# Optimization experiments

Measured on AMD Instinct MI355X. Metric: run time of the kernel, lower is better.

## Reference

```python
import jax, jax.numpy as jnp
import numpy as np

B_SZ, L, H, P = 8, 8192, 1024, 64  # batch, seq, d_inner, ssm_size
CONJ_SYM = True
DT_MIN, DT_MAX, DT_FLOOR = 1e-3, 1e-1, 1e-4


def setup_inputs() -> dict:
    key = jax.random.key(0)
    ks = jax.random.split(key, 8)
    u = jax.random.normal(ks[0], (B_SZ, L, H), dtype=jnp.float32)
    h_real = jnp.zeros((B_SZ, P), dtype=jnp.float32)
    h_imag = jnp.zeros((B_SZ, P), dtype=jnp.float32)
    # HiPPO-like stable init: Re(Lambda) = -0.5, Im(Lambda) = pi*k
    A_real = -0.5 * jnp.ones((P,), dtype=jnp.float32)
    A_imag = jnp.pi * jnp.arange(P, dtype=jnp.float32)
    local_P = 2 * P if CONJ_SYM else P
    b_scale = np.sqrt(1.0 / local_P).astype(np.float32)
    c_scale = np.sqrt(1.0 / H).astype(np.float32)
    B_real = jax.random.normal(ks[1], (P, H), dtype=jnp.float32) * b_scale
    B_imag = jax.random.normal(ks[2], (P, H), dtype=jnp.float32) * b_scale
    C_real = jax.random.normal(ks[3], (H, P), dtype=jnp.float32) * c_scale
    C_imag = jax.random.normal(ks[4], (H, P), dtype=jnp.float32) * c_scale
    D = jax.random.normal(ks[5], (H,), dtype=jnp.float32)
    # torch init: dt = exp(U(log dt_min, log dt_max)).clamp(dt_floor); inv_dt = dt + log(-expm1(-dt))
    log_dt = jax.random.uniform(ks[6], (P,), dtype=jnp.float32) \
        * (np.log(DT_MAX) - np.log(DT_MIN)) + np.log(DT_MIN)
    dt0 = jnp.clip(jnp.exp(log_dt), DT_FLOOR, None)
    inv_dt = dt0 + jnp.log(-jnp.expm1(-dt0))
    return {"u": u, "h_real": h_real, "h_imag": h_imag,
            "A_real": A_real, "A_imag": A_imag,
            "B_real": B_real, "B_imag": B_imag,
            "C_real": C_real, "C_imag": C_imag,
            "D": D, "inv_dt": inv_dt}


def reference(u, h_real, h_imag, A_real, A_imag, B_real, B_imag,
              C_real, C_imag, D, inv_dt):
    A = A_real + 1j * A_imag            # (P,)
    Bm = B_real + 1j * B_imag           # (P, H)
    Cm = C_real + 1j * C_imag           # (H, P)
    dt = jax.nn.softplus(inv_dt)        # step_rescale = 1.0
    # bilinear discretization
    den = 1.0 - (dt / 2.0) * A
    dA = (1.0 + (dt / 2.0) * A) / den   # (P,)
    dB = (dt / den)[:, None] * Bm       # (P, H)
    # input projection: Bu[b,l,p] = sum_h dB[p,h] * u[b,l,h]
    Bu = jnp.einsum('blh,ph->blp', u, dB)              # complex64 (B, L, P)
    h0 = h_real + 1j * h_imag                          # (B, P)
    Bu = Bu.at[:, 0].add(dA * h0)                      # fold initial state in
    a = jnp.broadcast_to(dA, Bu.shape)
    def combine(e1, e2):
        a1, b1 = e1
        a2, b2 = e2
        return a2 * a1, a2 * b1 + b2
    _, hs = jax.lax.associative_scan(combine, (a, Bu), axis=1)  # (B, L, P)
    yc = jnp.einsum('blp,hp->blh', hs, Cm)
    scale = 2.0 if CONJ_SYM else 1.0
    y = scale * yc.real + D * u
    h_last = hs[:, -1]
    return y, h_last.real, h_last.imag
```

## Files before the change

kernel.cpp:

```cpp
#include <hip/hip_runtime.h>

typedef unsigned short ushort_t;
typedef short s8v __attribute__((ext_vector_type(8)));
typedef unsigned short ushort8 __attribute__((ext_vector_type(8)));
typedef float floatx4 __attribute__((ext_vector_type(4)));

#define MFMA16(a, b, c) __builtin_amdgcn_mfma_f32_16x16x32_bf16((a), (b), (c), 0, 0, 0)

static constexpr int B_SZ = 8;
static constexpr int L = 8192;
static constexpr int H = 1024;
static constexpr int M_TOT = B_SZ * L;
static constexpr int S_CH = 128;
static constexpr int NC = L / S_CH;

__device__ inline ushort_t f2bf(float f) {
    union { float f; unsigned u; } v; v.f = f;
    unsigned r = v.u + 0x7fffu + ((v.u >> 16) & 1u);
    return (ushort_t)(r >> 16);
}

__global__ void params_kernel(const float* __restrict__ A_real,
                              const float* __restrict__ A_imag,
                              const float* __restrict__ inv_dt,
                              float* __restrict__ params,
                              float* __restrict__ dApow) {
    int p = threadIdx.x;
    float x = inv_dt[p];
    float dt = (x > 20.f) ? x : log1pf(expf(x));
    float ar = A_real[p], ai = A_imag[p];
    float dr = 1.f - 0.5f * dt * ar;
    float di = -0.5f * dt * ai;
    float inv = 1.f / fmaf(dr, dr, di * di);
    float nr = 1.f + 0.5f * dt * ar, ni = 0.5f * dt * ai;
    float dAr = (nr * dr + ni * di) * inv;
    float dAi = (ni * dr - nr * di) * inv;
    params[p]       = dAr;
    params[64 + p]  = dAi;
    params[128 + p] = dt * dr * inv;
    params[192 + p] = -dt * di * inv;
    float pr = 1.f, pi = 0.f;
    dApow[2 * p] = 1.f; dApow[2 * p + 1] = 0.f;
    for (int k = 1; k <= S_CH; k++) {
        float npr = pr * dAr - pi * dAi;
        float npi = pr * dAi + pi * dAr;
        pr = npr; pi = npi;
        dApow[k * 128 + 2 * p]     = pr;
        dApow[k * 128 + 2 * p + 1] = pi;
    }
}

__global__ void build_w(const float* __restrict__ Br, const float* __restrict__ Bi,
                        const float* __restrict__ Cr, const float* __restrict__ Ci,
                        const float* __restrict__ params,
                        ushort_t* __restrict__ W1T, ushort_t* __restrict__ CeffT) {
    int t = blockIdx.x * 256 + threadIdx.x;
    if (t < 128 * 1024) {
        int n = t >> 10, k = t & 1023;
        int p = n >> 1;
        float sr = params[128 + p], si = params[192 + p];
        float br = Br[p * 1024 + k], bi = Bi[p * 1024 + k];
        float v = (n & 1) ? (sr * bi + si * br) : (sr * br - si * bi);
        W1T[t] = f2bf(v);
    } else {
        int t2 = t - 128 * 1024;
        int h = t2 >> 7, k = t2 & 127;
        int p = k >> 1;
        float v = (k & 1) ? -2.f * Ci[h * 64 + p] : 2.f * Cr[h * 64 + p];
        CeffT[t2] = f2bf(v);
    }
}

__global__ __launch_bounds__(256) void gemm1s(const float* __restrict__ u,
                                              const ushort_t* __restrict__ W1T,
                                              const float* __restrict__ params,
                                              const float* __restrict__ dApow,
                                              float* __restrict__ hloc,
                                              float* __restrict__ endbuf) {
    __shared__ float bus[128 * 128];
    ushort_t* As = (ushort_t*)bus;
    ushort_t* Bs = As + 128 * 40;
    int tid = threadIdx.x;
    int wave = tid >> 6, lane = tid & 63;
    int q = lane >> 4, mn = lane & 15;
    size_t row0 = (size_t)blockIdx.x * 128;
    int r = tid >> 1, half = tid & 1;

    floatx4 acc[2][8] = {};

    for (int kk = 0; kk < 1024; kk += 32) {
        __syncthreads();
        {
            const float4* up = (const float4*)(u + (row0 + r) * 1024 + kk + half * 16);
            float4 f0 = up[0], f1 = up[1], f2 = up[2], f3 = up[3];
            ushort8 t0, t1;
            t0[0] = f2bf(f0.x); t0[1] = f2bf(f0.y); t0[2] = f2bf(f0.z); t0[3] = f2bf(f0.w);
            t0[4] = f2bf(f1.x); t0[5] = f2bf(f1.y); t0[6] = f2bf(f1.z); t0[7] = f2bf(f1.w);
            t1[0] = f2bf(f2.x); t1[1] = f2bf(f2.y); t1[2] = f2bf(f2.z); t1[3] = f2bf(f2.w);
            t1[4] = f2bf(f3.x); t1[5] = f2bf(f3.y); t1[6] = f2bf(f3.z); t1[7] = f2bf(f3.w);
            ushort8* dst = (ushort8*)&As[r * 40 + half * 16];
            dst[0] = t0; dst[1] = t1;
            const ushort8* wp = (const ushort8*)(W1T + r * 1024 + kk + half * 16);
            ushort8* db = (ushort8*)&Bs[r * 40 + half * 16];
            db[0] = wp[0]; db[1] = wp[1];
        }
        __syncthreads();
        s8v a0 = *(const s8v*)&As[(wave * 32 + mn) * 40 + q * 8];
        s8v a1 = *(const s8v*)&As[(wave * 32 + 16 + mn) * 40 + q * 8];
        #pragma unroll
        for (int j = 0; j < 8; j++) {
            s8v bf = *(const s8v*)&Bs[(j * 16 + mn) * 40 + q * 8];
            acc[0][j] = MFMA16(a0, bf, acc[0][j]);
            acc[1][j] = MFMA16(a1, bf, acc[1][j]);
        }
    }
    __syncthreads();
    #pragma unroll
    for (int i = 0; i < 2; i++)
        #pragma unroll
        for (int j = 0; j < 8; j++)
            #pragma unroll
            for (int reg = 0; reg < 4; reg++) {
                int row = wave * 32 + i * 16 + q * 4 + reg;
                bus[row * 128 + j * 16 + mn] = acc[i][j][reg];
            }
    __syncthreads();

    float dAr = params[lane], dAi = params[64 + lane];
    float hr = 0.f, hi = 0.f;
    int base = wave * 32 * 128 + 2 * lane;
    #pragma unroll 4
    for (int t = 0; t < 32; t++) {
        float2 v = *(float2*)&bus[base + t * 128];
        float nhr = fmaf(dAr, hr, fmaf(-dAi, hi, v.x));
        float nhi = fmaf(dAr, hi, fmaf(dAi, hr, v.y));
        hr = nhr; hi = nhi;
        *(float2*)&bus[base + t * 128] = make_float2(hr, hi);
    }
    __syncthreads();

    float a32r = dApow[32 * 128 + 2 * lane], a32i = dApow[32 * 128 + 2 * lane + 1];
    float cr = 0.f, ci = 0.f;
    for (int w2 = 0; w2 < wave; w2++) {
        float2 e = *(float2*)&bus[(w2 * 32 + 31) * 128 + 2 * lane];
        float tr = fmaf(a32r, cr, fmaf(-a32i, ci, e.x));
        float ti = fmaf(a32r, ci, fmaf(a32i, cr, e.y));
        cr = tr; ci = ti;
    }

    float* gbase = hloc + (row0 + wave * 32) * 128 + 2 * lane;
    float lr = 0.f, li = 0.f;
    #pragma unroll 4
    for (int t = 0; t < 32; t++) {
        float2 v = *(float2*)&bus[base + t * 128];
        float pr = dApow[(t + 1) * 128 + 2 * lane];
        float pi = dApow[(t + 1) * 128 + 2 * lane + 1];
        float orr = v.x + pr * cr - pi * ci;
        float oi  = v.y + pr * ci + pi * cr;
        *(float2*)(gbase + (size_t)t * 128) = make_float2(orr, oi);
        lr = orr; li = oi;
    }
    if (wave == 3) {
        float* e = endbuf + (size_t)blockIdx.x * 128 + 2 * lane;
        e[0] = lr; e[1] = li;
    }
}

__global__ void scan_carry(const float* __restrict__ endbuf,
                           const float* __restrict__ dApow,
                           const float* __restrict__ h0r,
                           const float* __restrict__ h0i,
                           float* __restrict__ carry) {
    int t = blockIdx.x * 64 + threadIdx.x;
    int b = t >> 6, p = t & 63;
    float aSr = dApow[S_CH * 128 + 2 * p], aSi = dApow[S_CH * 128 + 2 * p + 1];
    float cr = h0r[b * 64 + p], ci = h0i[b * 64 + p];
    for (int c = 0; c < NC; c++) {
        float* dst = carry + ((size_t)b * NC + c) * 128 + 2 * p;
        dst[0] = cr; dst[1] = ci;
        const float* e = endbuf + ((size_t)b * NC + c) * 128 + 2 * p;
        float er = e[0], ei = e[1];
        float nr = fmaf(aSr, cr, fmaf(-aSi, ci, er));
        float ni = fmaf(aSr, ci, fmaf(aSi, cr, ei));
        cr = nr; ci = ni;
    }
}

__global__ __launch_bounds__(256) void gemm2(const float* __restrict__ hloc,
                                             const ushort_t* __restrict__ CeffT,
                                             const float* __restrict__ u,
                                             const float* __restrict__ D,
                                             const float* __restrict__ dApow,
                                             const float* __restrict__ carry,
                                             float* __restrict__ y,
                                             float* __restrict__ out_hlast) {
    __shared__ ushort_t As[128][136];
    __shared__ ushort_t Bs[128][136];
    int tid = threadIdx.x;
    int wave = tid >> 6, lane = tid & 63;
    int q = lane >> 4, mn = lane & 15;
    size_t row0 = (size_t)blockIdx.x * 128;
    int r = tid >> 1, half = tid & 1;
    {
        size_t rrow = row0 + r;
        int b = (int)(rrow >> 13);
        int l = (int)(rrow & (L - 1));
        int c = l >> 7;
        int kp = (l & (S_CH - 1)) + 1;
        const float4* hp = (const float4*)(hloc + rrow * 128 + half * 64);
        const float4* pw = (const float4*)(dApow + (size_t)kp * 128 + half * 64);
        const float4* cv = (const float4*)(carry + ((size_t)b * NC + c) * 128 + half * 64);
        ushort8* dst = (ushort8*)&As[r][half * 64];
        bool last = (l == L - 1);
        #pragma unroll
        for (int j = 0; j < 8; j++) {
            float4 hv0 = hp[2 * j], hv1 = hp[2 * j + 1];
            float4 p0 = pw[2 * j], p1 = pw[2 * j + 1];
            float4 c0 = cv[2 * j], c1 = cv[2 * j + 1];
            float r0 = hv0.x + p0.x * c0.x - p0.y * c0.y;
            float i0 = hv0.y + p0.x * c0.y + p0.y * c0.x;
            float r1 = hv0.z + p0.z * c0.z - p0.w * c0.w;
            float i1 = hv0.w + p0.z * c0.w + p0.w * c0.z;
            float r2 = hv1.x + p1.x * c1.x - p1.y * c1.y;
            float i2 = hv1.y + p1.x * c1.y + p1.y * c1.x;
            float r3 = hv1.z + p1.z * c1.z - p1.w * c1.w;
            float i3 = hv1.w + p1.z * c1.w + p1.w * c1.z;
            ushort8 o;
            o[0] = f2bf(r0); o[1] = f2bf(i0); o[2] = f2bf(r1); o[3] = f2bf(i1);
            o[4] = f2bf(r2); o[5] = f2bf(i2); o[6] = f2bf(r3); o[7] = f2bf(i3);
            dst[j] = o;
            if (last) {
                int pb = (half * 64 + j * 8) >> 1;
                out_hlast[b * 64 + pb]           = r0; out_hlast[512 + b * 64 + pb]     = i0;
                out_hlast[b * 64 + pb + 1]       = r1; out_hlast[512 + b * 64 + pb + 1] = i1;
                out_hlast[b * 64 + pb + 2]       = r2; out_hlast[512 + b * 64 + pb + 2] = i2;
                out_hlast[b * 64 + pb + 3]       = r3; out_hlast[512 + b * 64 + pb + 3] = i3;
            }
        }
    }
    for (int ct = 0; ct < 8; ct++) {
        __syncthreads();
        {
            const ushort8* src = (const ushort8*)(CeffT + (size_t)(ct * 128 + r) * 128 + half * 64);
            ushort8* dst = (ushort8*)&Bs[r][half * 64];
            #pragma unroll
            for (int i = 0; i < 8; i++) dst[i] = src[i];
        }
        __syncthreads();
        floatx4 acc[2][8] = {};
        #pragma unroll
        for (int kk = 0; kk < 128; kk += 32) {
            s8v a0 = *(const s8v*)&As[wave * 32 + mn][kk + q * 8];
            s8v a1 = *(const s8v*)&As[wave * 32 + 16 + mn][kk + q * 8];
            #pragma unroll
            for (int j = 0; j < 8; j++) {
                s8v bf = *(const s8v*)&Bs[j * 16 + mn][kk + q * 8];
                acc[0][j] = MFMA16(a0, bf, acc[0][j]);
                acc[1][j] = MFMA16(a1, bf, acc[1][j]);
            }
        }
        float dv[8];
        #pragma unroll
        for (int j = 0; j < 8; j++) dv[j] = D[ct * 128 + j * 16 + mn];
        #pragma unroll
        for (int i = 0; i < 2; i++)
            #pragma unroll
            for (int j = 0; j < 8; j++) {
                int col = ct * 128 + j * 16 + mn;
                #pragma unroll
                for (int reg = 0; reg < 4; reg++) {
                    size_t row = row0 + wave * 32 + i * 16 + q * 4 + reg;
                    y[row * 1024 + col] = acc[i][j][reg] + dv[j] * u[row * 1024 + col];
                }
            }
    }
}

extern "C" void kernel_launch(void* const* d_in, const int* in_sizes, int n_in,
                              void* d_out, int out_size, void* d_ws, size_t ws_size,
                              hipStream_t stream) {
    const float* u      = (const float*)d_in[0];
    const float* h_r    = (const float*)d_in[1];
    const float* h_i    = (const float*)d_in[2];
    const float* A_real = (const float*)d_in[3];
    const float* A_imag = (const float*)d_in[4];
    const float* B_real = (const float*)d_in[5];
    const float* B_imag = (const float*)d_in[6];
    const float* C_real = (const float*)d_in[7];
    const float* C_imag = (const float*)d_in[8];
    const float* D      = (const float*)d_in[9];
    const float* inv_dt = (const float*)d_in[10];
    float* out = (float*)d_out;

    float* wsf       = (float*)d_ws;
    float* P_params  = wsf;
    float* P_dApow   = wsf + 1024;
    float* P_carry   = wsf + 1024 + 16640;
    float* P_end     = P_carry + 65536;
    ushort_t* P_W1T  = (ushort_t*)(P_end + 65536);
    ushort_t* P_Ceff = P_W1T + 128 * 1024;
    float* P_Bu      = (float*)(P_Ceff + 1024 * 128);

    params_kernel<<<1, 64, 0, stream>>>(A_real, A_imag, inv_dt, P_params, P_dApow);
    build_w<<<1024, 256, 0, stream>>>(B_real, B_imag, C_real, C_imag, P_params, P_W1T, P_Ceff);
    gemm1s<<<M_TOT / 128, 256, 0, stream>>>(u, P_W1T, P_params, P_dApow, P_Bu, P_end);
    scan_carry<<<8, 64, 0, stream>>>(P_end, P_dApow, h_r, h_i, P_carry);
    gemm2<<<M_TOT / 128, 256, 0, stream>>>(P_Bu, P_Ceff, u, D, P_dApow, P_carry,
                                           out, out + (size_t)M_TOT * H);
}
```

Measured before the change: 592.2 us.

## Stage GEMM weights via direct global-to-LDS loads with swizzled prepacked layout

Prepacks the W1T and CeffT weight matrices into a tiled, XOR-swizzled layout. Both GEMMs then bring them into a 64KB LDS buffer with global_load_lds in 4 phases instead of 32 or 8 small per-iteration stages. A-operands (u in gemm1, the corrected hidden state in gemm2) are loaded straight from global into registers and converted with packed bf16 conversion, so they no longer pass through LDS. This removes most barriers and LDS round-trips. The cost is higher register pressure, uncoalesced per-lane A loads, and larger LDS use that may cut occupancy.

```diff
diff --git a/kernel.cpp b/kernel.cpp
--- a/kernel.cpp
+++ b/kernel.cpp
@@ -18,6 +18,20 @@
     union { float f; unsigned u; } v; v.f = f;
     unsigned r = v.u + 0x7fffu + ((v.u >> 16) & 1u);
     return (ushort_t)(r >> 16);
+}
+
+__device__ inline unsigned cvtpk(float lo, float hi) {
+    unsigned r;
+    asm("v_cvt_pk_bf16_f32 %0, %1, %2" : "=v"(r) : "v"(lo), "v"(hi));
+    return r;
+}
+
+typedef union { s8v v; unsigned u[4]; } u32x4;
+
+__device__ inline void gload_lds16(const void* g, void* l) {
+    __builtin_amdgcn_global_load_lds(
+        (const __attribute__((address_space(1))) void*)g,
+        (__attribute__((address_space(3))) void*)l, 16, 0, 0);
 }
 
 __global__ void params_kernel(const float* __restrict__ A_real,
@@ -55,19 +69,39 @@
                         const float* __restrict__ params,
                         ushort_t* __restrict__ W1T, ushort_t* __restrict__ CeffT) {
     int t = blockIdx.x * 256 + threadIdx.x;
-    if (t < 128 * 1024) {
-        int n = t >> 10, k = t & 1023;
+    if (t < 16384) {
+        int ti = t >> 9, g = t & 511;
+        int n = g >> 2;
+        int qq = (g & 3) ^ ((n >> 1) & 3);
+        int kb = ti * 32 + qq * 8;
         int p = n >> 1;
         float sr = params[128 + p], si = params[192 + p];
-        float br = Br[p * 1024 + k], bi = Bi[p * 1024 + k];
-        float v = (n & 1) ? (sr * bi + si * br) : (sr * br - si * bi);
-        W1T[t] = f2bf(v);
+        ushort8 o;
+        #pragma unroll
+        for (int e = 0; e < 8; e++) {
+            int k = kb + e;
+            float br = Br[p * 1024 + k], bi = Bi[p * 1024 + k];
+            float v = (n & 1) ? (sr * bi + si * br) : (sr * br - si * bi);
+            o[e] = f2bf(v);
+        }
+        *(ushort8*)&W1T[t * 8] = o;
     } else {
-        int t2 = t - 128 * 1024;
-        int h = t2 >> 7, k = t2 & 127;
-        int p = k >> 1;
-        float v = (k & 1) ? -2.f * Ci[h * 64 + p] : 2.f * Cr[h * 64 + p];
-        CeffT[t2] = f2bf(v);
+        int t2 = t - 16384;
+        int ct_ti = t2 >> 9, g = t2 & 511;
+        int ct = ct_ti >> 2, ti = ct_ti & 3;
+        int n = g >> 2;
+        int h = ct * 128 + n;
+        int qq = (g & 3) ^ ((n >> 1) & 3);
+        int kb = ti * 32 + qq * 8;
+        ushort8 o;
+        #pragma unroll
+        for (int e = 0; e < 8; e++) {
+            int k = kb + e;
+            int p = k >> 1;
+            float v = (k & 1) ? -2.f * Ci[h * 64 + p] : 2.f * Cr[h * 64 + p];
+            o[e] = f2bf(v);
+        }
+        *(ushort8*)&CeffT[t2 * 8] = o;
     }
 }
 
@@ -77,41 +111,49 @@
                                               const float* __restrict__ dApow,
                                               float* __restrict__ hloc,
                                               float* __restrict__ endbuf) {
-    __shared__ float bus[128 * 128];
-    ushort_t* As = (ushort_t*)bus;
-    ushort_t* Bs = As + 128 * 40;
+    __shared__ ushort_t Blds[32768];
+    float* bus = (float*)Blds;
     int tid = threadIdx.x;
     int wave = tid >> 6, lane = tid & 63;
     int q = lane >> 4, mn = lane & 15;
+    int swz = q ^ ((mn >> 1) & 3);
     size_t row0 = (size_t)blockIdx.x * 128;
-    int r = tid >> 1, half = tid & 1;
+
+    const float* uA0 = u + (row0 + wave * 32 + mn) * 1024 + q * 8;
+    const float* uA1 = uA0 + 16 * 1024;
 
     floatx4 acc[2][8] = {};
 
-    for (int kk = 0; kk < 1024; kk += 32) {
+    for (int ph = 0; ph < 4; ph++) {
+        if (ph) __syncthreads();
+        {
+            const ushort_t* gsrc = W1T + (size_t)ph * 32768 + wave * 512 + lane * 8;
+            ushort_t* ldst = Blds + wave * 512;
+            #pragma unroll
+            for (int it = 0; it < 16; it++)
+                gload_lds16(gsrc + it * 2048, ldst + it * 2048);
+        }
         __syncthreads();
-        {
-            const float4* up = (const float4*)(u + (row0 + r) * 1024 + kk + half * 16);
-            float4 f0 = up[0], f1 = up[1], f2 = up[2], f3 = up[3];
-            ushort8 t0, t1;
-            t0[0] = f2bf(f0.x); t0[1] = f2bf(f0.y); t0[2] = f2bf(f0.z); t0[3] = f2bf(f0.w);
-            t0[4] = f2bf(f1.x); t0[5] = f2bf(f1.y); t0[6] = f2bf(f1.z); t0[7] = f2bf(f1.w);
-            t1[0] = f2bf(f2.x); t1[1] = f2bf(f2.y); t1[2] = f2bf(f2.z); t1[3] = f2bf(f2.w);
-            t1[4] = f2bf(f3.x); t1[5] = f2bf(f3.y); t1[6] = f2bf(f3.z); t1[7] = f2bf(f3.w);
-            ushort8* dst = (ushort8*)&As[r * 40 + half * 16];
-            dst[0] = t0; dst[1] = t1;
-            const ushort8* wp = (const ushort8*)(W1T + r * 1024 + kk + half * 16);
-            ushort8* db = (ushort8*)&Bs[r * 40 + half * 16];
-            db[0] = wp[0]; db[1] = wp[1];
-        }
-        __syncthreads();
-        s8v a0 = *(const s8v*)&As[(wave * 32 + mn) * 40 + q * 8];
-        s8v a1 = *(const s8v*)&As[(wave * 32 + 16 + mn) * 40 + q * 8];
-        #pragma unroll
-        for (int j = 0; j < 8; j++) {
-            s8v bf = *(const s8v*)&Bs[(j * 16 + mn) * 40 + q * 8];
-            acc[0][j] = MFMA16(a0, bf, acc[0][j]);
-            acc[1][j] = MFMA16(a1, bf, acc[1][j]);
+        const float* ua0 = uA0 + ph * 256;
+        const float* ua1 = uA1 + ph * 256;
+        #pragma unroll
+        for (int kt = 0; kt < 8; kt++) {
+            float4 f00 = *(const float4*)(ua0 + kt * 32);
+            float4 f01 = *(const float4*)(ua0 + kt * 32 + 4);
+            float4 f10 = *(const float4*)(ua1 + kt * 32);
+            float4 f11 = *(const float4*)(ua1 + kt * 32 + 4);
+            u32x4 pa0, pa1;
+            pa0.u[0] = cvtpk(f00.x, f00.y); pa0.u[1] = cvtpk(f00.z, f00.w);
+            pa0.u[2] = cvtpk(f01.x, f01.y); pa0.u[3] = cvtpk(f01.z, f01.w);
+            pa1.u[0] = cvtpk(f10.x, f10.y); pa1.u[1] = cvtpk(f10.z, f10.w);
+            pa1.u[2] = cvtpk(f11.x, f11.y); pa1.u[3] = cvtpk(f11.z, f11.w);
+            int bofs = kt * 4096 + swz * 8;
+            #pragma unroll
+            for (int j = 0; j < 8; j++) {
+                s8v bf = *(const s8v*)&Blds[bofs + (j * 16 + mn) * 32];
+                acc[0][j] = MFMA16(pa0.v, bf, acc[0][j]);
+                acc[1][j] = MFMA16(pa1.v, bf, acc[1][j]);
+            }
         }
     }
     __syncthreads();
@@ -129,7 +171,7 @@
     float dAr = params[lane], dAi = params[64 + lane];
     float hr = 0.f, hi = 0.f;
     int base = wave * 32 * 128 + 2 * lane;
-    #pragma unroll 4
+    #pragma unroll 8
     for (int t = 0; t < 32; t++) {
         float2 v = *(float2*)&bus[base + t * 128];
         float nhr = fmaf(dAr, hr, fmaf(-dAi, hi, v.x));
@@ -150,7 +192,7 @@
 
     float* gbase = hloc + (row0 + wave * 32) * 128 + 2 * lane;
     float lr = 0.f, li = 0.f;
-    #pragma unroll 4
+    #pragma unroll 8
     for (int t = 0; t < 32; t++) {
         float2 v = *(float2*)&bus[base + t * 128];
         float pr = dApow[(t + 1) * 128 + 2 * lane];
@@ -194,85 +236,92 @@
                                              const float* __restrict__ carry,
                                              float* __restrict__ y,
                                              float* __restrict__ out_hlast) {
-    __shared__ ushort_t As[128][136];
-    __shared__ ushort_t Bs[128][136];
+    __shared__ ushort_t Blds[32768];
     int tid = threadIdx.x;
     int wave = tid >> 6, lane = tid & 63;
     int q = lane >> 4, mn = lane & 15;
+    int swz = q ^ ((mn >> 1) & 3);
     size_t row0 = (size_t)blockIdx.x * 128;
-    int r = tid >> 1, half = tid & 1;
-    {
-        size_t rrow = row0 + r;
-        int b = (int)(rrow >> 13);
-        int l = (int)(rrow & (L - 1));
-        int c = l >> 7;
-        int kp = (l & (S_CH - 1)) + 1;
-        const float4* hp = (const float4*)(hloc + rrow * 128 + half * 64);
-        const float4* pw = (const float4*)(dApow + (size_t)kp * 128 + half * 64);
-        const float4* cv = (const float4*)(carry + ((size_t)b * NC + c) * 128 + half * 64);
-        ushort8* dst = (ushort8*)&As[r][half * 64];
-        bool last = (l == L - 1);
-        #pragma unroll
-        for (int j = 0; j < 8; j++) {
-            float4 hv0 = hp[2 * j], hv1 = hp[2 * j + 1];
-            float4 p0 = pw[2 * j], p1 = pw[2 * j + 1];
-            float4 c0 = cv[2 * j], c1 = cv[2 * j + 1];
-            float r0 = hv0.x + p0.x * c0.x - p0.y * c0.y;
-            float i0 = hv0.y + p0.x * c0.y + p0.y * c0.x;
-            float r1 = hv0.z + p0.z * c0.z - p0.w * c0.w;
-            float i1 = hv0.w + p0.z * c0.w + p0.w * c0.z;
-            float r2 = hv1.x + p1.x * c1.x - p1.y * c1.y;
-            float i2 = hv1.y + p1.x * c1.y + p1.y * c1.x;
-            float r3 = hv1.z + p1.z * c1.z - p1.w * c1.w;
-            float i3 = hv1.w + p1.z * c1.w + p1.w * c1.z;
-            ushort8 o;
-            o[0] = f2bf(r0); o[1] = f2bf(i0); o[2] = f2bf(r1); o[3] = f2bf(i1);
-            o[4] = f2bf(r2); o[5] = f2bf(i2); o[6] = f2bf(r3); o[7] = f2bf(i3);
-            dst[j] = o;
+    int b = blockIdx.x >> 6;
+    int c = blockIdx.x & 63;
+
+    u32x4 A[2][4];
+    #pragma unroll
+    for (int i = 0; i < 2; i++) {
+        int r_i = wave * 32 + i * 16 + mn;
+        int kp = r_i + 1;
+        const float* hrow = hloc + (row0 + r_i) * 128;
+        const float* prow = dApow + (size_t)kp * 128;
+        const float* crow = carry + ((size_t)b * NC + c) * 128;
+        bool last = (c == NC - 1) && (r_i == 127);
+        #pragma unroll
+        for (int kt = 0; kt < 4; kt++) {
+            int kb = kt * 32 + q * 8;
+            float4 h0 = *(const float4*)(hrow + kb);
+            float4 h1 = *(const float4*)(hrow + kb + 4);
+            float4 p0 = *(const float4*)(prow + kb);
+            float4 p1 = *(const float4*)(prow + kb + 4);
+            float4 c0 = *(const float4*)(crow + kb);
+            float4 c1 = *(const float4*)(crow + kb + 4);
+            float f0 = h0.x + p0.x * c0.x - p0.y * c0.y;
+            float f1 = h0.y + p0.x * c0.y + p0.y * c0.x;
+            float f2 = h0.z + p0.z * c0.z - p0.w * c0.w;
+            float f3 = h0.w + p0.z * c0.w + p0.w * c0.z;
+            float f4 = h1.x + p1.x * c1.x - p1.y * c1.y;
+            float f5 = h1.y + p1.x * c1.y + p1.y * c1.x;
+            float f6 = h1.z + p1.z * c1.z - p1.w * c1.w;
+            float f7 = h1.w + p1.z * c1.w + p1.w * c1.z;
+            A[i][kt].u[0] = cvtpk(f0, f1); A[i][kt].u[1] = cvtpk(f2, f3);
+            A[i][kt].u[2] = cvtpk(f4, f5); A[i][kt].u[3] = cvtpk(f6, f7);
             if (last) {
-                int pb = (half * 64 + j * 8) >> 1;
-                out_hlast[b * 64 + pb]           = r0; out_hlast[512 + b * 64 + pb]     = i0;
-                out_hlast[b * 64 + pb + 1]       = r1; out_hlast[512 + b * 64 + pb + 1] = i1;
-                out_hlast[b * 64 + pb + 2]       = r2; out_hlast[512 + b * 64 + pb + 2] = i2;
-                out_hlast[b * 64 + pb + 3]       = r3; out_hlast[512 + b * 64 + pb + 3] = i3;
+                int pb = kt * 16 + q * 4;
+                out_hlast[b * 64 + pb]           = f0; out_hlast[512 + b * 64 + pb]     = f1;
+                out_hlast[b * 64 + pb + 1]       = f2; out_hlast[512 + b * 64 + pb + 1] = f3;
+                out_hlast[b * 64 + pb + 2]       = f4; out_hlast[512 + b * 64 + pb + 2] = f5;
+                out_hlast[b * 64 + pb + 3]       = f6; out_hlast[512 + b * 64 + pb + 3] = f7;
             }
         }
     }
-    for (int ct = 0; ct < 8; ct++) {
+
+    for (int ph = 0; ph < 4; ph++) {
+        if (ph) __syncthreads();
+        {
+            const ushort_t* gsrc = CeffT + (size_t)ph * 32768 + wave * 512 + lane * 8;
+            ushort_t* ldst = Blds + wave * 512;
+            #pragma unroll
+            for (int it = 0; it < 16; it++)
+                gload_lds16(gsrc + it * 2048, ldst + it * 2048);
+        }
         __syncthreads();
-        {
-            const ushort8* src = (const ushort8*)(CeffT + (size_t)(ct * 128 + r) * 128 + half * 64);
-            ushort8* dst = (ushort8*)&Bs[r][half * 64];
-            #pragma unroll
-            for (int i = 0; i < 8; i++) dst[i] = src[i];
-        }
-        __syncthreads();
-        floatx4 acc[2][8] = {};
-        #pragma unroll
-        for (int kk = 0; kk < 128; kk += 32) {
-            s8v a0 = *(const s8v*)&As[wave * 32 + mn][kk + q * 8];
-            s8v a1 = *(const s8v*)&As[wave * 32 + 16 + mn][kk + q * 8];
-            #pragma unroll
-            for (int j = 0; j < 8; j++) {
-                s8v bf = *(const s8v*)&Bs[j * 16 + mn][kk + q * 8];
-                acc[0][j] = MFMA16(a0, bf, acc[0][j]);
-                acc[1][j] = MFMA16(a1, bf, acc[1][j]);
-            }
-        }
-        float dv[8];
-        #pragma unroll
-        for (int j = 0; j < 8; j++) dv[j] = D[ct * 128 + j * 16 + mn];
-        #pragma unroll
-        for (int i = 0; i < 2; i++)
-            #pragma unroll
-            for (int j = 0; j < 8; j++) {
-                int col = ct * 128 + j * 16 + mn;
+        #pragma unroll
+        for (int sub = 0; sub < 2; sub++) {
+            int ct = ph * 2 + sub;
+            floatx4 acc[2][8] = {};
+            #pragma unroll
+            for (int kt = 0; kt < 4; kt++) {
+                int bofs = (sub * 4 + kt) * 4096 + swz * 8;
                 #pragma unroll
-                for (int reg = 0; reg < 4; reg++) {
-                    size_t row = row0 + wave * 32 + i * 16 + q * 4 + reg;
-                    y[row * 1024 + col] = acc[i][j][reg] + dv[j] * u[row * 1024 + col];
+                for (int j = 0; j < 8; j++) {
+                    s8v bf = *(const s8v*)&Blds[bofs + (j * 16 + mn) * 32];
+                    acc[0][j] = MFMA16(A[0][kt].v, bf, acc[0][j]);
+                    acc[1][j] = MFMA16(A[1][kt].v, bf, acc[1][j]);
                 }
             }
+            float dv[8];
+            #pragma unroll
+            for (int j = 0; j < 8; j++) dv[j] = D[ct * 128 + j * 16 + mn];
+            #pragma unroll
+            for (int i = 0; i < 2; i++)
+                #pragma unroll
+                for (int j = 0; j < 8; j++) {
+                    int col = ct * 128 + j * 16 + mn;
+                    #pragma unroll
+                    for (int reg = 0; reg < 4; reg++) {
+                        size_t row = row0 + wave * 32 + i * 16 + q * 4 + reg;
+                        y[row * 1024 + col] = acc[i][j][reg] + dv[j] * u[row * 1024 + col];
+                    }
+                }
+        }
     }
 }
 
@@ -302,7 +351,7 @@
     float* P_Bu      = (float*)(P_Ceff + 1024 * 128);
 
     params_kernel<<<1, 64, 0, stream>>>(A_real, A_imag, inv_dt, P_params, P_dApow);
-    build_w<<<1024, 256, 0, stream>>>(B_real, B_imag, C_real, C_imag, P_params, P_W1T, P_Ceff);
+    build_w<<<128, 256, 0, stream>>>(B_real, B_imag, C_real, C_imag, P_params, P_W1T, P_Ceff);
     gemm1s<<<M_TOT / 128, 256, 0, stream>>>(u, P_W1T, P_params, P_dApow, P_Bu, P_end);
     scan_carry<<<8, 64, 0, stream>>>(P_end, P_dApow, h_r, h_i, P_carry);
     gemm2<<<M_TOT / 128, 256, 0, stream>>>(P_Bu, P_Ceff, u, D, P_dApow, P_carry,
```

After: 621.6 us. +5.0%, slower.
